# Performance work log

Hardware: AMD Instinct MI355X
Metric: run time of the kernel (lower is better)

## Reference

```python
import jax, jax.numpy as jnp
import numpy as np
from jax.scipy.special import gammaln

# dims
S, B, T, N = 8, 128, 256, 128      # samples, trials, time bins, neurons
L, Hh, Hd, Hl = 64, 128, 64, 128   # latent, backward-enc h, dynamics hidden, local-enc hidden


def kl_diag(m, P, mu, Q):
    # KL(N(m, diag P) || N(mu, diag Q)), summed over last dim
    return 0.5 * jnp.sum(jnp.log(Q) - jnp.log(P) + (P + (m - mu) ** 2) / Q - 1.0, axis=-1)


def setup_inputs() -> dict:
    key = jax.random.key(0)
    ks = jax.random.split(key, 12)
    g = lambda i, shape, s=0.1: s * jax.random.normal(ks[i], shape, dtype=jnp.float32)
    y = jax.random.randint(ks[0], (B, T, N), 0, 5).astype(jnp.float32)  # spike counts
    return dict(
        y=y, n_samples=S,
        W_be=g(1, (N, Hh)), b_be=jnp.zeros((Hh,), jnp.float32),
        W_ic=g(2, (Hh, 2 * L)), b_ic=jnp.zeros((2 * L,), jnp.float32),
        W_le1=g(3, (Hh + L, Hl)), b_le1=jnp.zeros((Hl,), jnp.float32),
        W_le2=g(4, (Hl, 2 * L)), b_le2=jnp.zeros((2 * L,), jnp.float32),
        W_dyn1=g(5, (L, Hd)), b_dyn1=jnp.zeros((Hd,), jnp.float32),
        W_dyn2=g(6, (Hd, L)), b_dyn2=jnp.zeros((L,), jnp.float32),
        C=g(7, (L, N)), b_c=jnp.full((N,), -1.0, jnp.float32),
        log_Q=jnp.full((L,), -2.0, jnp.float32),
        m_0=jnp.zeros((L,), jnp.float32),
        log_Q_0=jnp.zeros((L,), jnp.float32),
        eps0=jax.random.normal(ks[8], (S, B, L), dtype=jnp.float32),
        eps=jax.random.normal(ks[9], (T - 1, S, B, L), dtype=jnp.float32),
    )


def reference(y, n_samples, W_be, b_be, W_ic, b_ic, W_le1, b_le1, W_le2, b_le2,
              W_dyn1, b_dyn1, W_dyn2, b_dyn2, C, b_c, log_Q, m_0, log_Q_0, eps0, eps):
    Q = jax.nn.softplus(log_Q)
    Q0 = jax.nn.softplus(log_Q_0)

    # backward encoder: per-step MLP y -> h  [B,T,Hh]
    h = jnp.tanh(y @ W_be + b_be)

    # t = 0: init_c_encoder on h[:,0]
    mp0 = h[:, 0] @ W_ic + b_ic
    m0e, P0 = mp0[..., :L], jax.nn.softplus(mp0[..., L:])
    z0 = m0e + jnp.sqrt(P0) * eps0                       # [S,B,L]
    kl0 = kl_diag(m0e, P0, m_0, Q0)                      # [B]

    def mean_fn(z):
        return jnp.tanh(z @ W_dyn1 + b_dyn1) @ W_dyn2 + b_dyn2

    def step(z_prev, xs):
        h_t, eps_t = xs                                  # [B,Hh], [S,B,L]
        inp = jnp.concatenate(
            [jnp.broadcast_to(h_t, (n_samples,) + h_t.shape), z_prev], axis=-1)
        mp = jnp.tanh(inp @ W_le1 + b_le1) @ W_le2 + b_le2
        m_t, P_t = mp[..., :L], jax.nn.softplus(mp[..., L:])
        z_t = m_t + jnp.sqrt(P_t) * eps_t                # [S,B,L]
        kl_t = kl_diag(m_t, P_t, mean_fn(z_prev), Q).mean(axis=0)  # [B]
        return z_t, (z_t, kl_t)

    h_rest = jnp.swapaxes(h[:, 1:], 0, 1)                # [T-1,B,Hh]
    _, (z_rest, kl_rest) = jax.lax.scan(step, z0, (h_rest, eps))

    z = jnp.concatenate([z0[:, :, None], jnp.moveaxis(z_rest, 0, 2)], axis=2)  # [S,B,T,L]
    kl = jnp.concatenate([kl0[:, None], kl_rest.T], axis=1)                    # [B,T]

    # Poisson log-likelihood, summed over neurons, averaged over samples
    log_rate = z @ C + b_c                               # [S,B,T,N]
    ell = jnp.sum(y * log_rate - jnp.exp(log_rate) - gammaln(y + 1.0), axis=-1).mean(axis=0)  # [B,T]

    loss = (kl - ell).sum(axis=-1).mean()
    m_stat = z.mean(axis=0)                              # [B,T,L]
    return loss, z, m_stat
```

## Files before the change

### kernel.cpp

```cpp
#include <hip/hip_runtime.h>

constexpr int S = 8, B = 128, T = 256, N = 128;
constexpr int L = 64, Hh = 128, Hd = 64, Hl = 128;
constexpr int BT = B * T;

#define DEVFN __device__ __forceinline__

typedef float    f32x4_t __attribute__((ext_vector_type(4)));
typedef _Float16 f16x8_t __attribute__((ext_vector_type(8)));
typedef _Float16 f16x4_t __attribute__((ext_vector_type(4)));

DEVFN float softplus_f(float x) {
    return (x > 0.f) ? (x + log1pf(expf(-x))) : log1pf(expf(x));
}
DEVFN float softplus_fast(float x) {
    return fmaxf(x, 0.f) + __logf(1.f + __expf(-fabsf(x)));
}
DEVFN float fast_tanh(float x) {
    float ex = __builtin_exp2f(x * 2.885390081777927f);
    return 1.f - 2.f / (ex + 1.f);
}
DEVFN float gaOf(float yv) {
    int yi = (int)yv;
    return (yi < 2) ? 0.f
         : ((yi == 2) ? 0.6931471805599453f
         : ((yi == 3) ? 1.791759469228055f : 3.1780538303479458f));
}

__global__ __launch_bounds__(256) void kA(
        const float* __restrict__ y,
        const float* __restrict__ W_be, const float* __restrict__ b_be,
        const float* __restrict__ W_le1, const float* __restrict__ b_le1,
        float* __restrict__ A, float* __restrict__ h0) {
    __shared__ alignas(16) _Float16 yS[32][136];
    __shared__ alignas(16) _Float16 hS[32][152];
    __shared__ alignas(16) float    st[32][136];
    __shared__ float bbeS[128];

    const int tid = threadIdx.x;
    const int w = tid >> 6, l = tid & 63;
    const int lo = l & 15, hi = l >> 4;
    const int bt0 = blockIdx.x * 32;

    if (tid < 128) bbeS[tid] = b_be[tid];

    {
        const float4* y4 = (const float4*)(y + (size_t)bt0 * 128);
        #pragma unroll
        for (int k = 0; k < 4; ++k) {
            int i = k * 256 + tid;
            float4 v = y4[i];
            int row = i >> 5, c4 = (i & 31) * 4;
            f16x4_t h4;
            h4[0] = (_Float16)v.x; h4[1] = (_Float16)v.y;
            h4[2] = (_Float16)v.z; h4[3] = (_Float16)v.w;
            *(f16x4_t*)&yS[row][c4] = h4;
        }
    }

    f16x8_t awb[2][4], awa[2][4];
    #pragma unroll
    for (int ct = 0; ct < 2; ++ct)
        #pragma unroll
        for (int kt = 0; kt < 4; ++kt) {
            f16x8_t f, g;
            #pragma unroll
            for (int e = 0; e < 8; ++e) {
                size_t off = (size_t)(kt * 32 + 8 * hi + e) * 128 + (32 * w + 16 * ct + lo);
                f[e] = (_Float16)W_be[off];
                g[e] = (_Float16)W_le1[off];
            }
            awb[ct][kt] = f; awa[ct][kt] = g;
        }
    const f32x4_t bl0 = *(const f32x4_t*)&b_le1[32 * w + 4 * hi];
    const f32x4_t bl1 = *(const f32x4_t*)&b_le1[32 * w + 16 + 4 * hi];
    __syncthreads();

    #pragma unroll
    for (int rt = 0; rt < 2; ++rt) {
        f32x4_t acc0 = {0.f,0.f,0.f,0.f}, acc1 = {0.f,0.f,0.f,0.f};
        #pragma unroll
        for (int kt = 0; kt < 4; ++kt) {
            const f16x8_t bf = *(const f16x8_t*)&yS[16 * rt + lo][kt * 32 + 8 * hi];
            acc0 = __builtin_amdgcn_mfma_f32_16x16x32_f16(awb[0][kt], bf, acc0, 0, 0, 0);
            acc1 = __builtin_amdgcn_mfma_f32_16x16x32_f16(awb[1][kt], bf, acc1, 0, 0, 0);
        }
        *(f32x4_t*)&st[16 * rt + lo][32 * w + 4 * hi]      = acc0;
        *(f32x4_t*)&st[16 * rt + lo][32 * w + 16 + 4 * hi] = acc1;
    }
    __syncthreads();

    {
        const int trow = tid >> 3, cb = (tid & 7) * 16;
        const bool isH0 = ((bt0 & 255) == 0) && (trow == 0);
        float* h0p = h0 + (size_t)(bt0 >> 8) * 128;
        #pragma unroll
        for (int j = 0; j < 16; ++j) {
            float hv = fast_tanh(st[trow][cb + j] + bbeS[cb + j]);
            hS[trow][cb + j] = (_Float16)hv;
            if (isH0) h0p[cb + j] = hv;
        }
    }
    __syncthreads();

    #pragma unroll
    for (int rt = 0; rt < 2; ++rt) {
        f32x4_t acc0 = {0.f,0.f,0.f,0.f}, acc1 = {0.f,0.f,0.f,0.f};
        #pragma unroll
        for (int kt = 0; kt < 4; ++kt) {
            const f16x8_t bf = *(const f16x8_t*)&hS[16 * rt + lo][kt * 32 + 8 * hi];
            acc0 = __builtin_amdgcn_mfma_f32_16x16x32_f16(awa[0][kt], bf, acc0, 0, 0, 0);
            acc1 = __builtin_amdgcn_mfma_f32_16x16x32_f16(awa[1][kt], bf, acc1, 0, 0, 0);
        }
        acc0 += bl0; acc1 += bl1;
        float* Ar = A + (size_t)(bt0 + 16 * rt + lo) * 128;
        *(f32x4_t*)&Ar[32 * w + 4 * hi]      = acc0;
        *(f32x4_t*)&Ar[32 * w + 16 + 4 * hi] = acc1;
    }
}

__global__ __launch_bounds__(128) void kB(
        const float* __restrict__ h0, const float* __restrict__ W_ic,
        const float* __restrict__ b_ic, const float* __restrict__ m_0,
        const float* __restrict__ log_Q_0, const float* __restrict__ eps0,
        float* __restrict__ zout, float* __restrict__ kl0w) {
    __shared__ float hr[128];
    __shared__ float mp[128];
    const int b = blockIdx.x, tid = threadIdx.x;
    hr[tid] = h0[b * 128 + tid];
    __syncthreads();
    float acc = b_ic[tid];
    #pragma unroll 8
    for (int k = 0; k < 128; k++) acc += hr[k] * W_ic[k * 128 + tid];
    mp[tid] = acc;
    __syncthreads();

    float term = 0.f;
    if (tid < 64) {
        float m = mp[tid];
        float P = softplus_f(mp[tid + 64]);
        float sq = sqrtf(P);
        #pragma unroll
        for (int s = 0; s < 8; s++) {
            float e = eps0[((size_t)s * B + b) * 64 + tid];
            zout[(((size_t)s * B + b) * T + 0) * 64 + tid] = m + sq * e;
        }
        float Q0 = softplus_f(log_Q_0[tid]);
        float d = m - m_0[tid];
        term = 0.5f * (logf(Q0) - logf(P) + (P + d * d) / Q0 - 1.f);
    }
    #pragma unroll
    for (int off = 32; off; off >>= 1) term += __shfl_down(term, off);
    if (tid == 0) kl0w[b] = term;
}

__global__ __launch_bounds__(256) void kC(
        const float* __restrict__ Aglob,
        const float* __restrict__ W_le1, const float* __restrict__ W_le2,
        const float* __restrict__ b_le2,
        const float* __restrict__ W_dyn1, const float* __restrict__ b_dyn1,
        const float* __restrict__ W_dyn2, const float* __restrict__ b_dyn2,
        const float* __restrict__ log_Q, const float* __restrict__ eps,
        const float* __restrict__ Cmat, const float* __restrict__ b_c,
        const float* __restrict__ yglob,
        float* __restrict__ zout, float* __restrict__ kcl,
        float* __restrict__ kel) {
    __shared__ alignas(16) _Float16 zSm[16][88];
    __shared__ alignas(16) _Float16 hidS[16][152];
    __shared__ alignas(16) _Float16 gS[16][88];
    __shared__ alignas(16) float stH[2][136];
    __shared__ alignas(16) float stG[2][72];
    __shared__ alignas(16) float stM[2][136];
    __shared__ alignas(16) float stMU[2][72];
    __shared__ alignas(16) float stE[2][136];
    __shared__ float bmS[64], bpS[64], bmuS[64], bd1S[64], invQS[64];
    __shared__ float bcS[128];
    __shared__ float redK[4], redL[4];

    const int tid = threadIdx.x;
    const int b = blockIdx.x >> 2, sq = blockIdx.x & 3, s0 = sq * 2;
    const int w = tid >> 6, l = tid & 63;
    const int lo = l & 15, hi = l >> 4;
    const bool prod = (lo < 2);

    {
        _Float16* p1 = &zSm[0][0];
        _Float16* p2 = &hidS[0][0];
        _Float16* p3 = &gS[0][0];
        for (int i = tid; i < 16 * 88; i += 256) { p1[i] = (_Float16)0.f; p3[i] = (_Float16)0.f; }
        for (int i = tid; i < 16 * 152; i += 256) p2[i] = (_Float16)0.f;
    }
    if (tid < 64) {
        bmS[tid]   = b_le2[tid];
        bpS[tid]   = b_le2[64 + tid];
        bmuS[tid]  = b_dyn2[tid];
        bd1S[tid]  = b_dyn1[tid];
        invQS[tid] = 1.f / softplus_f(log_Q[tid]);
    }
    if (tid < 128) bcS[tid] = b_c[tid];

    f16x8_t a1[2][2], a2[2][4], a3[2], a4[2], aP[2][2];
    #pragma unroll
    for (int ct = 0; ct < 2; ++ct)
        #pragma unroll
        for (int kt = 0; kt < 2; ++kt) {
            f16x8_t f;
            #pragma unroll
            for (int e = 0; e < 8; ++e)
                f[e] = (_Float16)W_le1[(size_t)(128 + kt * 32 + 8 * hi + e) * 128 + (32 * w + 16 * ct + lo)];
            a1[ct][kt] = f;
        }
    #pragma unroll
    for (int ct = 0; ct < 2; ++ct) {
        const int col = (ct == 0 ? 16 * w : 64 + 16 * w) + lo;
        #pragma unroll
        for (int kt = 0; kt < 4; ++kt) {
            f16x8_t f;
            #pragma unroll
            for (int e = 0; e < 8; ++e)
                f[e] = (_Float16)W_le2[(size_t)(kt * 32 + 8 * hi + e) * 128 + col];
            a2[ct][kt] = f;
        }
    }
    #pragma unroll
    for (int kt = 0; kt < 2; ++kt) {
        f16x8_t f, g;
        #pragma unroll
        for (int e = 0; e < 8; ++e) {
            f[e] = (_Float16)W_dyn1[(size_t)(kt * 32 + 8 * hi + e) * 64 + (16 * w + lo)];
            g[e] = (_Float16)W_dyn2[(size_t)(kt * 32 + 8 * hi + e) * 64 + (16 * w + lo)];
        }
        a3[kt] = f; a4[kt] = g;
    }
    #pragma unroll
    for (int ct = 0; ct < 2; ++ct)
        #pragma unroll
        for (int kt = 0; kt < 2; ++kt) {
            f16x8_t f;
            #pragma unroll
            for (int e = 0; e < 8; ++e)
                f[e] = (_Float16)Cmat[(size_t)(kt * 32 + 8 * hi + e) * 128 + (32 * w + 16 * ct + lo)];
            aP[ct][kt] = f;
        }

    const int ha = l >> 5, hc = 32 * w + (l & 31);
    const int ga2 = (l >> 4) & 1, gc = 16 * w + (l & 15);
    const int es = ga2, ec = gc;
    const float* ap = Aglob + ((size_t)b * T + 1) * 128 + hc;
    const float* yp = yglob + ((size_t)b * T + 0) * 128 + hc;
    const float* ep = eps + (((size_t)(s0 + es)) * B + b) * 64 + ec;
    float*       zp = zout + ((((size_t)(s0 + es)) * B + b) * T + 1) * 64 + ec;

    float klAcc = 0.f;
    float ellAcc = 0.f;

    __syncthreads();
    if (tid < 128) {
        int ss = tid >> 6, c6 = tid & 63;
        zSm[ss][c6] = (_Float16)zout[(((size_t)(s0 + ss) * B + b) * T + 0) * 64 + c6];
    }
    __syncthreads();

    float aN = *ap;
    float yN = *yp;
    float eN = 0.f;
    if (l < 32) eN = *ep;

    for (int t = 1; t < T; ++t) {
        const float aC = aN, eC = eN, yC = yN;

        yp += 128; yN = *yp;
        if (t < T - 1) {
            ap += 128; aN = *ap;
            if (l < 32) { ep += (size_t)S * B * 64; eN = *ep; }
        }

        const f16x8_t bz0 = *(const f16x8_t*)&zSm[lo][8 * hi];
        const f16x8_t bz1 = *(const f16x8_t*)&zSm[lo][32 + 8 * hi];

        f32x4_t acc1a = {0.f,0.f,0.f,0.f}, acc1b = {0.f,0.f,0.f,0.f}, acc3 = {0.f,0.f,0.f,0.f};
        acc1a = __builtin_amdgcn_mfma_f32_16x16x32_f16(a1[0][0], bz0, acc1a, 0, 0, 0);
        acc1b = __builtin_amdgcn_mfma_f32_16x16x32_f16(a1[1][0], bz0, acc1b, 0, 0, 0);
        acc3  = __builtin_amdgcn_mfma_f32_16x16x32_f16(a3[0],    bz0, acc3,  0, 0, 0);
        acc1a = __builtin_amdgcn_mfma_f32_16x16x32_f16(a1[0][1], bz1, acc1a, 0, 0, 0);
        acc1b = __builtin_amdgcn_mfma_f32_16x16x32_f16(a1[1][1], bz1, acc1b, 0, 0, 0);
        acc3  = __builtin_amdgcn_mfma_f32_16x16x32_f16(a3[1],    bz1, acc3,  0, 0, 0);
        f32x4_t accE0 = {0.f,0.f,0.f,0.f}, accE1 = {0.f,0.f,0.f,0.f};
        accE0 = __builtin_amdgcn_mfma_f32_16x16x32_f16(aP[0][0], bz0, accE0, 0, 0, 0);
        accE1 = __builtin_amdgcn_mfma_f32_16x16x32_f16(aP[1][0], bz0, accE1, 0, 0, 0);
        accE0 = __builtin_amdgcn_mfma_f32_16x16x32_f16(aP[0][1], bz1, accE0, 0, 0, 0);
        accE1 = __builtin_amdgcn_mfma_f32_16x16x32_f16(aP[1][1], bz1, accE1, 0, 0, 0);

        if (prod) {
            *(f32x4_t*)&stH[lo][32 * w + 4 * hi]      = acc1a;
            *(f32x4_t*)&stH[lo][32 * w + 16 + 4 * hi] = acc1b;
            *(f32x4_t*)&stG[lo][16 * w + 4 * hi]      = acc3;
        }
        asm volatile("" ::: "memory");

        hidS[ha][hc] = (_Float16)fast_tanh(stH[ha][hc] + aC);
        if (l < 32)
            gS[ga2][gc] = (_Float16)fast_tanh(stG[ga2][gc] + bd1S[gc]);
        __syncthreads();

        const f16x8_t bh0 = *(const f16x8_t*)&hidS[lo][ 0 + 8 * hi];
        const f16x8_t bh1 = *(const f16x8_t*)&hidS[lo][32 + 8 * hi];
        const f16x8_t bh2 = *(const f16x8_t*)&hidS[lo][64 + 8 * hi];
        const f16x8_t bh3 = *(const f16x8_t*)&hidS[lo][96 + 8 * hi];
        const f16x8_t bg0 = *(const f16x8_t*)&gS[lo][8 * hi];
        const f16x8_t bg1 = *(const f16x8_t*)&gS[lo][32 + 8 * hi];

        f32x4_t accm = {0.f,0.f,0.f,0.f}, accp = {0.f,0.f,0.f,0.f}, acc4 = {0.f,0.f,0.f,0.f};
        accm = __builtin_amdgcn_mfma_f32_16x16x32_f16(a2[0][0], bh0, accm, 0, 0, 0);
        accp = __builtin_amdgcn_mfma_f32_16x16x32_f16(a2[1][0], bh0, accp, 0, 0, 0);
        acc4 = __builtin_amdgcn_mfma_f32_16x16x32_f16(a4[0],    bg0, acc4, 0, 0, 0);
        accm = __builtin_amdgcn_mfma_f32_16x16x32_f16(a2[0][1], bh1, accm, 0, 0, 0);
        accp = __builtin_amdgcn_mfma_f32_16x16x32_f16(a2[1][1], bh1, accp, 0, 0, 0);
        acc4 = __builtin_amdgcn_mfma_f32_16x16x32_f16(a4[1],    bg1, acc4, 0, 0, 0);
        accm = __builtin_amdgcn_mfma_f32_16x16x32_f16(a2[0][2], bh2, accm, 0, 0, 0);
        accp = __builtin_amdgcn_mfma_f32_16x16x32_f16(a2[1][2], bh2, accp, 0, 0, 0);
        accm = __builtin_amdgcn_mfma_f32_16x16x32_f16(a2[0][3], bh3, accm, 0, 0, 0);
        accp = __builtin_amdgcn_mfma_f32_16x16x32_f16(a2[1][3], bh3, accp, 0, 0, 0);

        if (prod) {
            *(f32x4_t*)&stE[lo][32 * w + 4 * hi]      = accE0;
            *(f32x4_t*)&stE[lo][32 * w + 16 + 4 * hi] = accE1;
        }
        asm volatile("" ::: "memory");
        {
            float lr = stE[ha][hc] + bcS[hc];
            ellAcc += 0.125f * (yC * lr - __expf(lr));
            if (sq == 0 && ha == 0) ellAcc -= gaOf(yC);
        }

        if (prod) {
            *(f32x4_t*)&stM[lo][16 * w + 4 * hi]       = accm;
            *(f32x4_t*)&stM[lo][64 + 16 * w + 4 * hi]  = accp;
            *(f32x4_t*)&stMU[lo][16 * w + 4 * hi]      = acc4;
        }
        asm volatile("" ::: "memory");

        if (l < 32) {
            float m  = stM[es][ec] + bmS[ec];
            float P  = softplus_fast(stM[es][64 + ec] + bpS[ec]);
            float mu = stMU[es][ec] + bmuS[ec];
            float iq = invQS[ec];
            float z  = m + sqrtf(P) * eC;
            *zp = z; zp += 64;
            zSm[es][ec] = (_Float16)z;
            float d = m - mu;
            klAcc += (P + d * d) * iq - __logf(P * iq) - 1.f;
        }
        __syncthreads();
    }

    {
        const f16x8_t bz0 = *(const f16x8_t*)&zSm[lo][8 * hi];
        const f16x8_t bz1 = *(const f16x8_t*)&zSm[lo][32 + 8 * hi];
        f32x4_t accE0 = {0.f,0.f,0.f,0.f}, accE1 = {0.f,0.f,0.f,0.f};
        accE0 = __builtin_amdgcn_mfma_f32_16x16x32_f16(aP[0][0], bz0, accE0, 0, 0, 0);
        accE1 = __builtin_amdgcn_mfma_f32_16x16x32_f16(aP[1][0], bz0, accE1, 0, 0, 0);
        accE0 = __builtin_amdgcn_mfma_f32_16x16x32_f16(aP[0][1], bz1, accE0, 0, 0, 0);
        accE1 = __builtin_amdgcn_mfma_f32_16x16x32_f16(aP[1][1], bz1, accE1, 0, 0, 0);
        if (prod) {
            *(f32x4_t*)&stE[lo][32 * w + 4 * hi]      = accE0;
            *(f32x4_t*)&stE[lo][32 * w + 16 + 4 * hi] = accE1;
        }
        asm volatile("" ::: "memory");
        float lr = stE[ha][hc] + bcS[hc];
        ellAcc += 0.125f * (yN * lr - __expf(lr));
        if (sq == 0 && ha == 0) ellAcc -= gaOf(yN);
    }

    float kv = klAcc;
    kv += __shfl_down(kv, 16);
    kv += __shfl_down(kv, 8);
    kv += __shfl_down(kv, 4);
    kv += __shfl_down(kv, 2);
    kv += __shfl_down(kv, 1);
    float ev = ellAcc;
    ev += __shfl_down(ev, 32);
    ev += __shfl_down(ev, 16);
    ev += __shfl_down(ev, 8);
    ev += __shfl_down(ev, 4);
    ev += __shfl_down(ev, 2);
    ev += __shfl_down(ev, 1);
    if (l == 0) { redK[w] = kv; redL[w] = ev; }
    __syncthreads();
    if (tid == 0) {
        kcl[blockIdx.x] = 0.0625f * (redK[0] + redK[1] + redK[2] + redK[3]);
        kel[blockIdx.x] = redL[0] + redL[1] + redL[2] + redL[3];
    }
}

__global__ __launch_bounds__(256) void kM(
        const float* __restrict__ zin, float* __restrict__ ms) {
    const int idx = blockIdx.x * 256 + threadIdx.x;
    const float4* z4 = (const float4*)zin;
    float4 acc = {0.f, 0.f, 0.f, 0.f};
    #pragma unroll
    for (int s = 0; s < 8; s++) {
        float4 v = z4[(size_t)s * BT * 16 + idx];
        acc.x += v.x; acc.y += v.y; acc.z += v.z; acc.w += v.w;
    }
    acc.x *= 0.125f; acc.y *= 0.125f; acc.z *= 0.125f; acc.w *= 0.125f;
    ((float4*)ms)[idx] = acc;
}

__global__ __launch_bounds__(256) void kR(
        const float* __restrict__ kl0w, const float* __restrict__ kcl,
        const float* __restrict__ kel, float* __restrict__ out0) {
    __shared__ float red4[4];
    const int tid = threadIdx.x;
    float acc = 0.f;
    #pragma unroll
    for (int ii = 0; ii < 2; ii++) {
        int i = tid + ii * 256;
        acc += kcl[i] - kel[i];
    }
    if (tid < 128) acc += kl0w[tid];
    #pragma unroll
    for (int off = 32; off; off >>= 1) acc += __shfl_down(acc, off);
    if ((tid & 63) == 0) red4[tid >> 6] = acc;
    __syncthreads();
    if (tid == 0) out0[0] = (red4[0] + red4[1] + red4[2] + red4[3]) * (1.0f / B);
}

extern "C" void kernel_launch(void* const* d_in, const int* in_sizes, int n_in,
                              void* d_out, int out_size, void* d_ws, size_t ws_size,
                              hipStream_t stream) {
    const float* y      = (const float*)d_in[0];
    const float* W_be   = (const float*)d_in[2];
    const float* b_be   = (const float*)d_in[3];
    const float* W_ic   = (const float*)d_in[4];
    const float* b_ic   = (const float*)d_in[5];
    const float* W_le1  = (const float*)d_in[6];
    const float* b_le1  = (const float*)d_in[7];
    const float* W_le2  = (const float*)d_in[8];
    const float* b_le2  = (const float*)d_in[9];
    const float* W_dyn1 = (const float*)d_in[10];
    const float* b_dyn1 = (const float*)d_in[11];
    const float* W_dyn2 = (const float*)d_in[12];
    const float* b_dyn2 = (const float*)d_in[13];
    const float* C      = (const float*)d_in[14];
    const float* b_c    = (const float*)d_in[15];
    const float* log_Q  = (const float*)d_in[16];
    const float* m_0    = (const float*)d_in[17];
    const float* log_Q_0= (const float*)d_in[18];
    const float* eps0   = (const float*)d_in[19];
    const float* eps    = (const float*)d_in[20];

    float* out = (float*)d_out;
    float* zo  = out + 1;
    float* ms  = out + 1 + (size_t)S * B * T * L;

    float* ws   = (float*)d_ws;
    float* kl0w = ws;
    float* kcl  = kl0w + B;
    float* kel  = kcl + 512;
    float* h0   = kel + 512;
    float* A    = h0 + (size_t)B * 128;

    kA<<<1024, 256, 0, stream>>>(y, W_be, b_be, W_le1, b_le1, A, h0);
    kB<<<128, 128, 0, stream>>>(h0, W_ic, b_ic, m_0, log_Q_0, eps0, zo, kl0w);
    kC<<<512, 256, 0, stream>>>(A, W_le1, W_le2, b_le2, W_dyn1, b_dyn1,
                                W_dyn2, b_dyn2, log_Q, eps, C, b_c, y,
                                zo, kcl, kel);
    kM<<<2048, 256, 0, stream>>>(zo, ms);
    kR<<<1, 256, 0, stream>>>(kl0w, kcl, kel, out);
}
```

Before: 392.4 us.

## Move Poisson likelihood out of recurrent scan into separate kernel fused with mean

Removes the per-step emission MFMAs, y loads and likelihood math from the sequential scan kernel, shortening its critical path. A new kernel reads back z after the scan, recomputes log-rates with MFMA, accumulates the Poisson likelihood and also writes the sample-mean statistic, replacing the separate mean kernel. This trades extra global reads of z for a lighter serial loop and one fewer launch.

New measurement: 343.6 us. 12.4% less time.

```diff
diff --git a/kernel.cpp b/kernel.cpp
--- a/kernel.cpp
+++ b/kernel.cpp
@@ -161,10 +161,7 @@
         const float* __restrict__ W_dyn1, const float* __restrict__ b_dyn1,
         const float* __restrict__ W_dyn2, const float* __restrict__ b_dyn2,
         const float* __restrict__ log_Q, const float* __restrict__ eps,
-        const float* __restrict__ Cmat, const float* __restrict__ b_c,
-        const float* __restrict__ yglob,
-        float* __restrict__ zout, float* __restrict__ kcl,
-        float* __restrict__ kel) {
+        float* __restrict__ zout, float* __restrict__ kcl) {
     __shared__ alignas(16) _Float16 zSm[16][88];
     __shared__ alignas(16) _Float16 hidS[16][152];
     __shared__ alignas(16) _Float16 gS[16][88];
@@ -172,10 +169,8 @@
     __shared__ alignas(16) float stG[2][72];
     __shared__ alignas(16) float stM[2][136];
     __shared__ alignas(16) float stMU[2][72];
-    __shared__ alignas(16) float stE[2][136];
     __shared__ float bmS[64], bpS[64], bmuS[64], bd1S[64], invQS[64];
-    __shared__ float bcS[128];
-    __shared__ float redK[4], redL[4];
+    __shared__ float redK[4];
 
     const int tid = threadIdx.x;
     const int b = blockIdx.x >> 2, sq = blockIdx.x & 3, s0 = sq * 2;
@@ -197,9 +192,8 @@
         bd1S[tid]  = b_dyn1[tid];
         invQS[tid] = 1.f / softplus_f(log_Q[tid]);
     }
-    if (tid < 128) bcS[tid] = b_c[tid];
-
-    f16x8_t a1[2][2], a2[2][4], a3[2], a4[2], aP[2][2];
+
+    f16x8_t a1[2][2], a2[2][4], a3[2], a4[2];
     #pragma unroll
     for (int ct = 0; ct < 2; ++ct)
         #pragma unroll
@@ -232,27 +226,15 @@
         }
         a3[kt] = f; a4[kt] = g;
     }
-    #pragma unroll
-    for (int ct = 0; ct < 2; ++ct)
-        #pragma unroll
-        for (int kt = 0; kt < 2; ++kt) {
-            f16x8_t f;
-            #pragma unroll
-            for (int e = 0; e < 8; ++e)
-                f[e] = (_Float16)Cmat[(size_t)(kt * 32 + 8 * hi + e) * 128 + (32 * w + 16 * ct + lo)];
-            aP[ct][kt] = f;
-        }
 
     const int ha = l >> 5, hc = 32 * w + (l & 31);
     const int ga2 = (l >> 4) & 1, gc = 16 * w + (l & 15);
     const int es = ga2, ec = gc;
     const float* ap = Aglob + ((size_t)b * T + 1) * 128 + hc;
-    const float* yp = yglob + ((size_t)b * T + 0) * 128 + hc;
     const float* ep = eps + (((size_t)(s0 + es)) * B + b) * 64 + ec;
     float*       zp = zout + ((((size_t)(s0 + es)) * B + b) * T + 1) * 64 + ec;
 
     float klAcc = 0.f;
-    float ellAcc = 0.f;
 
     __syncthreads();
     if (tid < 128) {
@@ -262,14 +244,12 @@
     __syncthreads();
 
     float aN = *ap;
-    float yN = *yp;
     float eN = 0.f;
     if (l < 32) eN = *ep;
 
     for (int t = 1; t < T; ++t) {
-        const float aC = aN, eC = eN, yC = yN;
-
-        yp += 128; yN = *yp;
+        const float aC = aN, eC = eN;
+
         if (t < T - 1) {
             ap += 128; aN = *ap;
             if (l < 32) { ep += (size_t)S * B * 64; eN = *ep; }
@@ -285,11 +265,6 @@
         acc1a = __builtin_amdgcn_mfma_f32_16x16x32_f16(a1[0][1], bz1, acc1a, 0, 0, 0);
         acc1b = __builtin_amdgcn_mfma_f32_16x16x32_f16(a1[1][1], bz1, acc1b, 0, 0, 0);
         acc3  = __builtin_amdgcn_mfma_f32_16x16x32_f16(a3[1],    bz1, acc3,  0, 0, 0);
-        f32x4_t accE0 = {0.f,0.f,0.f,0.f}, accE1 = {0.f,0.f,0.f,0.f};
-        accE0 = __builtin_amdgcn_mfma_f32_16x16x32_f16(aP[0][0], bz0, accE0, 0, 0, 0);
-        accE1 = __builtin_amdgcn_mfma_f32_16x16x32_f16(aP[1][0], bz0, accE1, 0, 0, 0);
-        accE0 = __builtin_amdgcn_mfma_f32_16x16x32_f16(aP[0][1], bz1, accE0, 0, 0, 0);
-        accE1 = __builtin_amdgcn_mfma_f32_16x16x32_f16(aP[1][1], bz1, accE1, 0, 0, 0);
 
         if (prod) {
             *(f32x4_t*)&stH[lo][32 * w + 4 * hi]      = acc1a;
@@ -323,17 +298,6 @@
         accp = __builtin_amdgcn_mfma_f32_16x16x32_f16(a2[1][3], bh3, accp, 0, 0, 0);
 
         if (prod) {
-            *(f32x4_t*)&stE[lo][32 * w + 4 * hi]      = accE0;
-            *(f32x4_t*)&stE[lo][32 * w + 16 + 4 * hi] = accE1;
-        }
-        asm volatile("" ::: "memory");
-        {
-            float lr = stE[ha][hc] + bcS[hc];
-            ellAcc += 0.125f * (yC * lr - __expf(lr));
-            if (sq == 0 && ha == 0) ellAcc -= gaOf(yC);
-        }
-
-        if (prod) {
             *(f32x4_t*)&stM[lo][16 * w + 4 * hi]       = accm;
             *(f32x4_t*)&stM[lo][64 + 16 * w + 4 * hi]  = accp;
             *(f32x4_t*)&stMU[lo][16 * w + 4 * hi]      = acc4;
@@ -354,30 +318,103 @@
         __syncthreads();
     }
 
-    {
-        const f16x8_t bz0 = *(const f16x8_t*)&zSm[lo][8 * hi];
-        const f16x8_t bz1 = *(const f16x8_t*)&zSm[lo][32 + 8 * hi];
-        f32x4_t accE0 = {0.f,0.f,0.f,0.f}, accE1 = {0.f,0.f,0.f,0.f};
-        accE0 = __builtin_amdgcn_mfma_f32_16x16x32_f16(aP[0][0], bz0, accE0, 0, 0, 0);
-        accE1 = __builtin_amdgcn_mfma_f32_16x16x32_f16(aP[1][0], bz0, accE1, 0, 0, 0);
-        accE0 = __builtin_amdgcn_mfma_f32_16x16x32_f16(aP[0][1], bz1, accE0, 0, 0, 0);
-        accE1 = __builtin_amdgcn_mfma_f32_16x16x32_f16(aP[1][1], bz1, accE1, 0, 0, 0);
-        if (prod) {
-            *(f32x4_t*)&stE[lo][32 * w + 4 * hi]      = accE0;
-            *(f32x4_t*)&stE[lo][32 * w + 16 + 4 * hi] = accE1;
-        }
-        asm volatile("" ::: "memory");
-        float lr = stE[ha][hc] + bcS[hc];
-        ellAcc += 0.125f * (yN * lr - __expf(lr));
-        if (sq == 0 && ha == 0) ellAcc -= gaOf(yN);
-    }
-
     float kv = klAcc;
     kv += __shfl_down(kv, 16);
     kv += __shfl_down(kv, 8);
     kv += __shfl_down(kv, 4);
     kv += __shfl_down(kv, 2);
     kv += __shfl_down(kv, 1);
+    if (l == 0) redK[w] = kv;
+    __syncthreads();
+    if (tid == 0)
+        kcl[blockIdx.x] = 0.0625f * (redK[0] + redK[1] + redK[2] + redK[3]);
+}
+
+__global__ __launch_bounds__(256) void kP2(
+        const float* __restrict__ zin, const float* __restrict__ Cmat,
+        const float* __restrict__ b_c, const float* __restrict__ yglob,
+        float* __restrict__ m_stat, float* __restrict__ kel) {
+    __shared__ alignas(16) _Float16 zP[16][72];
+    __shared__ alignas(16) float yP[256];
+    __shared__ float red4[4];
+
+    const int tid = threadIdx.x;
+    const int w = tid >> 6, l = tid & 63;
+    const int lo = l & 15, hi = l >> 4;
+    const int b = blockIdx.x >> 2, tq = blockIdx.x & 3;
+    const int tbase = tq * 64;
+
+    f16x8_t aC[2][2];
+    #pragma unroll
+    for (int ct = 0; ct < 2; ++ct)
+        #pragma unroll
+        for (int kt = 0; kt < 2; ++kt) {
+            f16x8_t f;
+            #pragma unroll
+            for (int e = 0; e < 8; ++e)
+                f[e] = (_Float16)Cmat[(size_t)(kt * 32 + 8 * hi + e) * 128 + (32 * w + 16 * ct + lo)];
+            aC[ct][kt] = f;
+        }
+    f32x4_t bc[2];
+    #pragma unroll
+    for (int ct = 0; ct < 2; ++ct)
+        #pragma unroll
+        for (int r = 0; r < 4; ++r)
+            bc[ct][r] = b_c[32 * w + 16 * ct + 4 * hi + r];
+
+    float ellAcc = 0.f;
+
+    for (int j = 0; j < 32; ++j) {
+        const int t0 = tbase + 2 * j;
+        __syncthreads();
+        {
+            int i = tid;
+            int s = i >> 5, rem = i & 31;
+            int tdx = rem >> 4, l4 = (rem & 15) * 4;
+            f32x4_t v = *(const f32x4_t*)&zin[(((size_t)s * B + b) * T + t0 + tdx) * 64 + l4];
+            f16x4_t h4;
+            h4[0] = (_Float16)v[0]; h4[1] = (_Float16)v[1];
+            h4[2] = (_Float16)v[2]; h4[3] = (_Float16)v[3];
+            *(f16x4_t*)&zP[s * 2 + tdx][l4] = h4;
+            yP[tid] = yglob[((size_t)b * T + t0) * 128 + tid];
+        }
+        __syncthreads();
+
+        if (tid < 128) {
+            int tdx = tid >> 6, ll = tid & 63;
+            float acc = 0.f;
+            #pragma unroll
+            for (int s = 0; s < 8; ++s) acc += (float)zP[s * 2 + tdx][ll];
+            m_stat[((size_t)b * T + t0 + tdx) * 64 + ll] = 0.125f * acc;
+        }
+
+        const f16x8_t bz0 = *(const f16x8_t*)&zP[lo][8 * hi];
+        const f16x8_t bz1 = *(const f16x8_t*)&zP[lo][32 + 8 * hi];
+        f32x4_t acc0 = {0.f,0.f,0.f,0.f}, acc1 = {0.f,0.f,0.f,0.f};
+        acc0 = __builtin_amdgcn_mfma_f32_16x16x32_f16(aC[0][0], bz0, acc0, 0, 0, 0);
+        acc1 = __builtin_amdgcn_mfma_f32_16x16x32_f16(aC[1][0], bz0, acc1, 0, 0, 0);
+        acc0 = __builtin_amdgcn_mfma_f32_16x16x32_f16(aC[0][1], bz1, acc0, 0, 0, 0);
+        acc1 = __builtin_amdgcn_mfma_f32_16x16x32_f16(aC[1][1], bz1, acc1, 0, 0, 0);
+
+        {
+            const int tdx = lo & 1;
+            float te = 0.f;
+            #pragma unroll
+            for (int r = 0; r < 4; ++r) {
+                int n0 = 32 * w + 4 * hi + r;
+                float lr0 = acc0[r] + bc[0][r];
+                float yv0 = yP[tdx * 128 + n0];
+                te += yv0 * lr0 - __expf(lr0);
+                int n1 = n0 + 16;
+                float lr1 = acc1[r] + bc[1][r];
+                float yv1 = yP[tdx * 128 + n1];
+                te += yv1 * lr1 - __expf(lr1);
+                if (lo < 2) te -= 8.f * (gaOf(yv0) + gaOf(yv1));
+            }
+            ellAcc += 0.125f * te;
+        }
+    }
+
     float ev = ellAcc;
     ev += __shfl_down(ev, 32);
     ev += __shfl_down(ev, 16);
@@ -385,26 +422,9 @@
     ev += __shfl_down(ev, 4);
     ev += __shfl_down(ev, 2);
     ev += __shfl_down(ev, 1);
-    if (l == 0) { redK[w] = kv; redL[w] = ev; }
-    __syncthreads();
-    if (tid == 0) {
-        kcl[blockIdx.x] = 0.0625f * (redK[0] + redK[1] + redK[2] + redK[3]);
-        kel[blockIdx.x] = redL[0] + redL[1] + redL[2] + redL[3];
-    }
-}
-
-__global__ __launch_bounds__(256) void kM(
-        const float* __restrict__ zin, float* __restrict__ ms) {
-    const int idx = blockIdx.x * 256 + threadIdx.x;
-    const float4* z4 = (const float4*)zin;
-    float4 acc = {0.f, 0.f, 0.f, 0.f};
-    #pragma unroll
-    for (int s = 0; s < 8; s++) {
-        float4 v = z4[(size_t)s * BT * 16 + idx];
-        acc.x += v.x; acc.y += v.y; acc.z += v.z; acc.w += v.w;
-    }
-    acc.x *= 0.125f; acc.y *= 0.125f; acc.z *= 0.125f; acc.w *= 0.125f;
-    ((float4*)ms)[idx] = acc;
+    if (l == 0) red4[w] = ev;
+    __syncthreads();
+    if (tid == 0) kel[blockIdx.x] = red4[0] + red4[1] + red4[2] + red4[3];
 }
 
 __global__ __launch_bounds__(256) void kR(
@@ -464,8 +484,7 @@
     kA<<<1024, 256, 0, stream>>>(y, W_be, b_be, W_le1, b_le1, A, h0);
     kB<<<128, 128, 0, stream>>>(h0, W_ic, b_ic, m_0, log_Q_0, eps0, zo, kl0w);
     kC<<<512, 256, 0, stream>>>(A, W_le1, W_le2, b_le2, W_dyn1, b_dyn1,
-                                W_dyn2, b_dyn2, log_Q, eps, C, b_c, y,
-                                zo, kcl, kel);
-    kM<<<2048, 256, 0, stream>>>(zo, ms);
+                                W_dyn2, b_dyn2, log_Q, eps, zo, kcl);
+    kP2<<<512, 256, 0, stream>>>(zo, C, b_c, y, ms, kel);
     kR<<<1, 256, 0, stream>>>(kl0w, kcl, kel, out);
 }
```
